# Optimization experiments

Hardware: AMD Instinct MI355X
Metric: run time of the kernel (lower is better)

The kernel has to match this reference:

```python
import jax, jax.numpy as jnp
import numpy as np

D, M, N = 1024, 16, 16384
H = D // M  # head dim = 64
C = 10.0    # tanh logit clipping


def setup_inputs() -> dict:
    key = jax.random.key(0)
    kb, kq, km, k1, k2, k3, k4 = jax.random.split(key, 7)
    def xavier(k, shape):
        # torch xavier_uniform: fan_in = prod(shape[1:]), fan_out = shape[0]*prod(shape[2:])
        fan_in = int(np.prod(shape[1:]))
        fan_out = shape[0] * int(np.prod(shape[2:]))
        bound = float(np.sqrt(6.0 / (fan_in + fan_out)))
        return jax.random.uniform(k, shape, jnp.float32, -bound, bound)
    return {
        "b": jax.random.normal(kb, (N, D), jnp.float32),
        "q_s_bar": jax.random.normal(kq, (D,), jnp.float32),
        "mask": jax.random.randint(km, (N,), 0, 2).astype(bool),
        "W_k_bar": xavier(k1, (M, H, D)),
        "W_v_bar": xavier(k2, (M, H, D)),
        "W_k": xavier(k3, (D, D)),
        "W_q": xavier(k4, (D, D)),
    }


def reference(b, q_s_bar, mask, W_k_bar, W_v_bar, W_k, W_q):
    # k_bar, v_bar: (N, M, H)  == matmul(W, b.t()).permute(2,0,1)
    k_bar = jnp.einsum('mhd,nd->nmh', W_k_bar, b)
    v_bar = jnp.einsum('mhd,nd->nmh', W_v_bar, b)
    k = b @ W_k.T                      # (N, D) == matmul(W_k, b.t()).t()
    q = q_s_bar.reshape(M, H)          # (M, H)
    # c_bar: (N, M, M) == matmul(k_bar, q.T) / sqrt(h)
    c_bar = jnp.einsum('nmh,gh->nmg', k_bar, q) / np.float32(np.sqrt(H))
    scores = jnp.where(mask[:, None, None], c_bar, -jnp.inf)
    attn = jax.nn.softmax(scores, axis=0)          # softmax over N
    # (N,M,M) @ (N,M,H) batched -> (N,M,H); view(N,-1).sum(0) -> (D,)
    q_s = jnp.einsum('nmg,ngh->nmh', attn, v_bar).reshape(N, D).sum(0)
    c = (k @ (W_q @ q_s)) / np.float32(np.sqrt(D))  # (N,)
    c = C * jnp.tanh(c)
    return jnp.where(mask, c, -jnp.inf)
```

## Files before the change

### kernel.cpp

```cpp
#include <hip/hip_runtime.h>
#include <math.h>
#include <float.h>

#define NN 16384
#define DD 1024
#define MM 16
#define HH 64
#define MG 256

typedef __attribute__((ext_vector_type(8))) short bh8;
typedef __attribute__((ext_vector_type(4))) float f32x4;

__device__ inline float bf2f(unsigned short u) {
    union { unsigned int i; float f; } v;
    v.i = ((unsigned int)u) << 16;
    return v.f;
}

__device__ inline unsigned short f2bf(float f) {
    union { float f; unsigned int i; } v;
    v.f = f;
    unsigned int r = v.i + 0x7FFFu + ((v.i >> 16) & 1u);
    return (unsigned short)(r >> 16);
}

__device__ inline float ld1(const void* p, long i, int isf) {
    return isf ? ((const float*)p)[i] : bf2f(((const unsigned short*)p)[i]);
}

__device__ inline float4 ld4(const void* p, long i, int isf) {
    if (isf) return *(const float4*)((const float*)p + i);
    ushort4 u = *(const ushort4*)((const unsigned short*)p + i);
    return make_float4(bf2f(u.x), bf2f(u.y), bf2f(u.z), bf2f(u.w));
}

__device__ inline bool get_mask(const unsigned char* mp, int n, int flag) {
    return flag ? (mp[n] != 0) : (mp[4 * n] != 0);
}

__device__ inline void gl_lds16(const void* g, void* l) {
    __builtin_amdgcn_global_load_lds(
        (const __attribute__((address_space(1))) unsigned int*)g,
        (__attribute__((address_space(3))) unsigned int*)l, 16, 0, 0);
}

__global__ void detect(const unsigned char* __restrict__ mp,
                       const unsigned char* __restrict__ bb, int* flags,
                       float* __restrict__ u, float* __restrict__ T) {
    int i = blockIdx.x * 256 + threadIdx.x;
    if (i < DD) u[i] = 0.f;
    float4 z = make_float4(0.f, 0.f, 0.f, 0.f);
#pragma unroll
    for (int j = 0; j < 4; j++) *(float4*)&T[(j * 16384 + i) * 4] = z;
    int v1 = ((i & 3) != 0 && mp[i] != 0) ? 1 : 0;
    unsigned char c = bb[4 * i + 1];
    bool expish = (c == 0x00) || (c == 0x80) || (c >= 0x30 && c <= 0x47) ||
                  (c >= 0xB0 && c <= 0xC7);
    int v2 = expish ? 0 : 1;
    unsigned long long b1 = __ballot(v1);
    unsigned long long b2 = __ballot(v2);
    if ((threadIdx.x & 63) == 0) {
        if (b1) atomicOr(&flags[0], 1);
        if (b2) atomicOr(&flags[1], 1);
    }
}

__global__ void fold_k(const void* __restrict__ Wkb, const void* __restrict__ qsb,
                       unsigned short* __restrict__ Abf, const int* __restrict__ flags) {
    __shared__ float q[DD];
    int isf = flags[1];
    int m = blockIdx.x;
    int d = blockIdx.y * 128 + threadIdx.x;
    for (int i = threadIdx.x; i < DD; i += 128) q[i] = ld1(qsb, i, isf);
    __syncthreads();
    float acc[MM];
#pragma unroll
    for (int g = 0; g < MM; g++) acc[g] = 0.f;
    for (int h = 0; h < HH; h++) {
        float w = ld1(Wkb, (long)(m * HH + h) * DD + d, isf);
#pragma unroll
        for (int g = 0; g < MM; g++) acc[g] += w * q[g * HH + h];
    }
#pragma unroll
    for (int g = 0; g < MM; g++)
        Abf[(long)(m * MM + g) * DD + d] = f2bf(acc[g] * 0.125f);
}

__global__ __launch_bounds__(256) void cvt_b(const void* __restrict__ bB,
                                             unsigned short* __restrict__ bbf,
                                             unsigned short* __restrict__ bT,
                                             const int* __restrict__ flags) {
    __shared__ unsigned short tl[2][32 * 68];
    const int isf = flags[1];
    const int t = threadIdx.x;
    const int n0 = blockIdx.x * 32;
    const int r = t >> 3, c8 = (t & 7) * 8;
    const int dT = t >> 2, ch = t & 3;
    const long gbase = (long)(n0 + r) * DD + c8;

    float cur[8], nxt[8];
    auto LOAD = [&](float* dst, int dt) {
        if (isf) {
            float4 v0 = *(const float4*)((const float*)bB + gbase + dt * 64);
            float4 v1 = *(const float4*)((const float*)bB + gbase + dt * 64 + 4);
            dst[0] = v0.x; dst[1] = v0.y; dst[2] = v0.z; dst[3] = v0.w;
            dst[4] = v1.x; dst[5] = v1.y; dst[6] = v1.z; dst[7] = v1.w;
        } else {
            bh8 v = *(const bh8*)((const unsigned short*)bB + gbase + dt * 64);
#pragma unroll
            for (int j = 0; j < 8; j++) dst[j] = bf2f((unsigned short)v[j]);
        }
    };

    LOAD(cur, 0);
#pragma unroll
    for (int dt = 0; dt < 16; dt++) {
        if (dt < 15) LOAD(nxt, dt + 1);
        bh8 o;
#pragma unroll
        for (int j = 0; j < 8; j++) o[j] = (short)f2bf(cur[j]);
        *(bh8*)&bbf[gbase + dt * 64] = o;
        unsigned short* row = &tl[dt & 1][r * 68 + c8];
        ushort4 lo, hi;
        lo.x = (unsigned short)o[0]; lo.y = (unsigned short)o[1];
        lo.z = (unsigned short)o[2]; lo.w = (unsigned short)o[3];
        hi.x = (unsigned short)o[4]; hi.y = (unsigned short)o[5];
        hi.z = (unsigned short)o[6]; hi.w = (unsigned short)o[7];
        *(ushort4*)row = lo;
        *(ushort4*)(row + 4) = hi;
        __syncthreads();
        bh8 y;
#pragma unroll
        for (int k = 0; k < 8; k++)
            y[k] = (short)tl[dt & 1][(ch * 8 + k) * 68 + dT];
        *(bh8*)&bT[(long)(dt * 64 + dT) * NN + n0 + ch * 8] = y;
#pragma unroll
        for (int j = 0; j < 8; j++) cur[j] = nxt[j];
    }
}

__global__ __launch_bounds__(256) void gemm_b_mfma(
    const unsigned short* __restrict__ Abf, const unsigned short* __restrict__ bbf,
    const unsigned char* __restrict__ mp, const int* __restrict__ flags,
    unsigned short* __restrict__ Cb) {
    __shared__ __align__(16) unsigned short As[128 * 64];
    __shared__ __align__(16) unsigned short Bs[64 * 64];
    int m0 = blockIdx.x * 128, n0 = blockIdx.y * 64;
    int t = threadIdx.x;
    int lane = t & 63, w = t >> 6;
    int wm = w >> 1, wn = w & 1;
    int r = lane & 15, q = lane >> 4;
    f32x4 acc[4][2] = {};
    for (int k0 = 0; k0 < DD; k0 += 64) {
#pragma unroll
        for (int i = 0; i < 4; i++) {
            int L = (i * 4 + w) * 64 + lane;
            int row = L >> 3, c = (L & 7) ^ (row & 7);
            gl_lds16(&Abf[(long)(m0 + row) * DD + k0 + c * 8], &As[(i * 4 + w) * 512]);
        }
#pragma unroll
        for (int i = 0; i < 2; i++) {
            int L = (i * 4 + w) * 64 + lane;
            int row = L >> 3, c = (L & 7) ^ (row & 7);
            gl_lds16(&bbf[(long)(n0 + row) * DD + k0 + c * 8], &Bs[(i * 4 + w) * 512]);
        }
        __syncthreads();
#pragma unroll
        for (int h = 0; h < 2; h++) {
            bh8 af[4], bfr[2];
#pragma unroll
            for (int fi = 0; fi < 4; fi++) {
                int row = wm * 64 + fi * 16 + r;
                int ck = (h * 4 + q) ^ (row & 7);
                af[fi] = *(const bh8*)&As[row * 64 + ck * 8];
            }
#pragma unroll
            for (int fj = 0; fj < 2; fj++) {
                int row = wn * 32 + fj * 16 + r;
                int ck = (h * 4 + q) ^ (row & 7);
                bfr[fj] = *(const bh8*)&Bs[row * 64 + ck * 8];
            }
#pragma unroll
            for (int fi = 0; fi < 4; fi++)
#pragma unroll
                for (int fj = 0; fj < 2; fj++)
                    acc[fi][fj] = __builtin_amdgcn_mfma_f32_16x16x32_bf16(
                        af[fi], bfr[fj], acc[fi][fj], 0, 0, 0);
        }
        __syncthreads();
    }
    int mflag = flags[0];
#pragma unroll
    for (int fj = 0; fj < 2; fj++) {
        int gn = n0 + wn * 32 + fj * 16 + r;
        float nb = get_mask(mp, gn, mflag) ? 0.f : -INFINITY;
#pragma unroll
        for (int fi = 0; fi < 4; fi++)
#pragma unroll
            for (int reg = 0; reg < 4; reg++) {
                int gm = m0 + wm * 64 + fi * 16 + q * 4 + reg;
                Cb[(long)gm * NN + gn] = f2bf(acc[fi][fj][reg] + nb);
            }
    }
}

__global__ __launch_bounds__(256) void softmax_f(const unsigned short* __restrict__ Cb,
                                                 unsigned short* __restrict__ P) {
    __shared__ float red[8];
    int mg = blockIdx.x, t = threadIdx.x;
    long base = (long)mg * NN;
    bh8 v[8];
#pragma unroll
    for (int j = 0; j < 8; j++) v[j] = *(const bh8*)&Cb[base + (j * 256 + t) * 8];
    float mx = -INFINITY;
#pragma unroll
    for (int j = 0; j < 8; j++)
#pragma unroll
        for (int e = 0; e < 8; e++) mx = fmaxf(mx, bf2f((unsigned short)v[j][e]));
#pragma unroll
    for (int off = 32; off; off >>= 1) mx = fmaxf(mx, __shfl_xor(mx, off, 64));
    if ((t & 63) == 0) red[t >> 6] = mx;
    __syncthreads();
    mx = fmaxf(fmaxf(red[0], red[1]), fmaxf(red[2], red[3]));
    float mxs = (mx == -INFINITY) ? 0.f : mx;
    float sm = 0.f;
#pragma unroll
    for (int j = 0; j < 8; j++)
#pragma unroll
        for (int e = 0; e < 8; e++) sm += expf(bf2f((unsigned short)v[j][e]) - mxs);
#pragma unroll
    for (int off = 32; off; off >>= 1) sm += __shfl_xor(sm, off, 64);
    if ((t & 63) == 0) red[4 + (t >> 6)] = sm;
    __syncthreads();
    sm = red[4] + red[5] + red[6] + red[7];
    float inv = (sm > 0.f) ? 1.0f / sm : 0.f;
#pragma unroll
    for (int j = 0; j < 8; j++) {
        bh8 o;
#pragma unroll
        for (int e = 0; e < 8; e++)
            o[e] = (short)f2bf(expf(bf2f((unsigned short)v[j][e]) - mxs) * inv);
        *(bh8*)&P[base + (j * 256 + t) * 8] = o;
    }
}

__global__ __launch_bounds__(256) void gemm_d_mfma(
    const unsigned short* __restrict__ P, const unsigned short* __restrict__ bT,
    float* __restrict__ T) {
    __shared__ __align__(16) unsigned short As[128 * 64];
    __shared__ __align__(16) unsigned short Bs[64 * 64];
    int m0 = blockIdx.x * 128, d0 = blockIdx.y * 64;
    long kbase = (long)blockIdx.z * 1024;
    int t = threadIdx.x;
    int lane = t & 63, w = t >> 6;
    int wm = w >> 1, wn = w & 1;
    int r = lane & 15, q = lane >> 4;
    f32x4 acc[4][2] = {};
    for (int k0 = 0; k0 < 1024; k0 += 64) {
#pragma unroll
        for (int i = 0; i < 4; i++) {
            int L = (i * 4 + w) * 64 + lane;
            int row = L >> 3, c = (L & 7) ^ (row & 7);
            gl_lds16(&P[(long)(m0 + row) * NN + kbase + k0 + c * 8], &As[(i * 4 + w) * 512]);
        }
#pragma unroll
        for (int i = 0; i < 2; i++) {
            int L = (i * 4 + w) * 64 + lane;
            int row = L >> 3, c = (L & 7) ^ (row & 7);
            gl_lds16(&bT[(long)(d0 + row) * NN + kbase + k0 + c * 8], &Bs[(i * 4 + w) * 512]);
        }
        __syncthreads();
#pragma unroll
        for (int h = 0; h < 2; h++) {
            bh8 af[4], bfr[2];
#pragma unroll
            for (int fi = 0; fi < 4; fi++) {
                int row = wm * 64 + fi * 16 + r;
                int ck = (h * 4 + q) ^ (row & 7);
                af[fi] = *(const bh8*)&As[row * 64 + ck * 8];
            }
#pragma unroll
            for (int fj = 0; fj < 2; fj++) {
                int row = wn * 32 + fj * 16 + r;
                int ck = (h * 4 + q) ^ (row & 7);
                bfr[fj] = *(const bh8*)&Bs[row * 64 + ck * 8];
            }
#pragma unroll
            for (int fi = 0; fi < 4; fi++)
#pragma unroll
                for (int fj = 0; fj < 2; fj++)
                    acc[fi][fj] = __builtin_amdgcn_mfma_f32_16x16x32_bf16(
                        af[fi], bfr[fj], acc[fi][fj], 0, 0, 0);
        }
        __syncthreads();
    }
#pragma unroll
    for (int fi = 0; fi < 4; fi++)
#pragma unroll
        for (int fj = 0; fj < 2; fj++)
#pragma unroll
            for (int reg = 0; reg < 4; reg++) {
                int gm = m0 + wm * 64 + fi * 16 + q * 4 + reg;
                int gd = d0 + wn * 32 + fj * 16 + r;
                atomicAdd(&T[(long)gm * DD + gd], acc[fi][fj][reg]);
            }
}

__global__ void fold_v(const void* __restrict__ Wvb, const float* __restrict__ T,
                       float* __restrict__ qs, const int* __restrict__ flags) {
    int isf = flags[1];
    int w = threadIdx.x >> 6, lane = threadIdx.x & 63;
    int o = blockIdx.x * 4 + w;
    int m = o >> 6, h = o & 63;
    float s = 0.f;
    for (int g = 0; g < MM; g++) {
        const float* Trow = T + (long)(m * MM + g) * DD;
        long wbase = (long)(g * HH + h) * DD;
#pragma unroll
        for (int k = 0; k < 4; k++) {
            int d = lane * 4 + k * 256;
            float4 tv = *(const float4*)&Trow[d];
            float4 wv = ld4(Wvb, wbase + d, isf);
            s += wv.x * tv.x + wv.y * tv.y + wv.z * tv.z + wv.w * tv.w;
        }
    }
    for (int off = 32; off; off >>= 1) s += __shfl_down(s, off, 64);
    if (lane == 0) qs[o] = s;
}

__global__ void matvec_rows(const void* __restrict__ W, const float* __restrict__ x,
                            float* __restrict__ y, const int* __restrict__ flags) {
    int isf = flags[1];
    int lane = threadIdx.x & 63;
    int r = blockIdx.x * 4 + (threadIdx.x >> 6);
    long base = (long)r * DD;
    float s = 0.f;
#pragma unroll
    for (int k = 0; k < 4; k++) {
        int j = lane * 4 + k * 256;
        float4 wv = ld4(W, base + j, isf);
        float4 xv = *(const float4*)&x[j];
        s += wv.x * xv.x + wv.y * xv.y + wv.z * xv.z + wv.w * xv.w;
    }
    for (int off = 32; off; off >>= 1) s += __shfl_down(s, off, 64);
    if (lane == 0) y[r] = s;
}

__global__ void matvec_col(const void* __restrict__ Wk, const float* __restrict__ w1,
                           float* __restrict__ u, const int* __restrict__ flags) {
    __shared__ float xs[16];
    int isf = flags[1];
    int d = blockIdx.x * 256 + threadIdx.x;
    int i0 = blockIdx.y * 16;
    if (threadIdx.x < 16) xs[threadIdx.x] = w1[i0 + threadIdx.x];
    __syncthreads();
    float s = 0.f;
#pragma unroll
    for (int ii = 0; ii < 16; ii++) s += ld1(Wk, (long)(i0 + ii) * DD + d, isf) * xs[ii];
    atomicAdd(&u[d], s);
}

__global__ void final_k(const unsigned short* __restrict__ bbf, const float* __restrict__ u,
                        const unsigned char* __restrict__ mp, const int* __restrict__ flags,
                        void* __restrict__ out) {
    int mflag = flags[0];
    int isf = flags[1];
    int n = blockIdx.x * 4 + (threadIdx.x >> 6);
    int lane = threadIdx.x & 63;
    const unsigned short* row = bbf + (long)n * DD;
    float s = 0.f;
#pragma unroll
    for (int k = 0; k < 4; k++) {
        int j = lane * 4 + k * 256;
        ushort4 v = *(const ushort4*)&row[j];
        float4 uu = *(const float4*)&u[j];
        s += bf2f(v.x) * uu.x + bf2f(v.y) * uu.y + bf2f(v.z) * uu.z + bf2f(v.w) * uu.w;
    }
    for (int off = 32; off; off >>= 1) s += __shfl_down(s, off, 64);
    if (lane == 0) {
        float c = 10.f * tanhf(s * (1.0f / 32.0f));
        bool mk = get_mask(mp, n, mflag);
        if (isf) {
            union { unsigned int i; float f; } vv;
            vv.i = mk ? (((unsigned int)f2bf(c)) << 16) : 0xFF7F0000u;
            ((float*)out)[n] = vv.f;
        } else {
            ((unsigned short*)out)[n] = mk ? f2bf(c) : (unsigned short)0xFF7F;
        }
    }
}

extern "C" void kernel_launch(void* const* d_in, const int* in_sizes, int n_in,
                              void* d_out, int out_size, void* d_ws, size_t ws_size,
                              hipStream_t stream) {
    const void* b = d_in[0];
    const void* qsb = d_in[1];
    const unsigned char* mp = (const unsigned char*)d_in[2];
    const void* Wkb = d_in[3];
    const void* Wvb = d_in[4];
    const void* Wk = d_in[5];
    const void* Wq = d_in[6];

    char* ws = (char*)d_ws;
    unsigned short* bbf = (unsigned short*)(ws);
    unsigned short* bT = (unsigned short*)(ws + (32u << 20));
    unsigned short* Cb = (unsigned short*)(ws + (64u << 20));
    unsigned short* P = (unsigned short*)(ws + (80u << 20));
    unsigned short* Abf = (unsigned short*)(ws + (88u << 20));
    float* T = (float*)(ws + (89u << 20));
    float* small = (float*)(ws + (90u << 20));
    float* qs = small;
    float* w1 = qs + 1024;
    float* u = w1 + 1024;
    int* flags = (int*)(u + 1024);

    hipMemsetAsync(flags, 0, 2 * sizeof(int), stream);

    detect<<<64, 256, 0, stream>>>(mp, (const unsigned char*)b, flags, u, T);
    fold_k<<<dim3(16, 8), 128, 0, stream>>>(Wkb, qsb, Abf, flags);
    cvt_b<<<512, 256, 0, stream>>>(b, bbf, bT, flags);
    gemm_b_mfma<<<dim3(2, 256), 256, 0, stream>>>(Abf, bbf, mp, flags, Cb);
    softmax_f<<<256, 256, 0, stream>>>(Cb, P);
    gemm_d_mfma<<<dim3(2, 16, 16), 256, 0, stream>>>(P, bT, T);
    fold_v<<<256, 256, 0, stream>>>(Wvb, T, qs, flags);
    matvec_rows<<<256, 256, 0, stream>>>(Wq, qs, w1, flags);
    matvec_col<<<dim3(4, 64), 256, 0, stream>>>(Wk, w1, u, flags);
    final_k<<<4096, 256, 0, stream>>>(bbf, u, mp, flags, d_out);
}
```

Measured before the change: 231.9 us.

## Double-buffer GEMM LDS tiles, split-K partials with reduce, wider softmax blocks

Both MFMA GEMMs now use two LDS buffers and issue the next k-tile's global-to-LDS loads before computing on the current tile, so memory latency can overlap with MFMA work. The split-K GEMM writes per-split partial results into a 16-slice buffer, and a new reduce kernel sums them. This replaces float atomics and removes the need to zero T in detect. Softmax now runs with 512 threads per row so each thread holds half as many registers. The cost is an extra kernel launch, a 16 MB partial buffer that must be written and read back, and twice the LDS per GEMM block, which may lower occupancy.

```diff
diff --git a/kernel.cpp b/kernel.cpp
--- a/kernel.cpp
+++ b/kernel.cpp
@@ -46,12 +46,9 @@
 
 __global__ void detect(const unsigned char* __restrict__ mp,
                        const unsigned char* __restrict__ bb, int* flags,
-                       float* __restrict__ u, float* __restrict__ T) {
+                       float* __restrict__ u) {
     int i = blockIdx.x * 256 + threadIdx.x;
     if (i < DD) u[i] = 0.f;
-    float4 z = make_float4(0.f, 0.f, 0.f, 0.f);
-#pragma unroll
-    for (int j = 0; j < 4; j++) *(float4*)&T[(j * 16384 + i) * 4] = z;
     int v1 = ((i & 3) != 0 && mp[i] != 0) ? 1 : 0;
     unsigned char c = bb[4 * i + 1];
     bool expish = (c == 0x00) || (c == 0x80) || (c >= 0x30 && c <= 0x47) ||
@@ -143,28 +140,35 @@
     const unsigned short* __restrict__ Abf, const unsigned short* __restrict__ bbf,
     const unsigned char* __restrict__ mp, const int* __restrict__ flags,
     unsigned short* __restrict__ Cb) {
-    __shared__ __align__(16) unsigned short As[128 * 64];
-    __shared__ __align__(16) unsigned short Bs[64 * 64];
+    __shared__ __align__(16) unsigned short As[2][128 * 64];
+    __shared__ __align__(16) unsigned short Bs[2][64 * 64];
     int m0 = blockIdx.x * 128, n0 = blockIdx.y * 64;
     int t = threadIdx.x;
     int lane = t & 63, w = t >> 6;
     int wm = w >> 1, wn = w & 1;
     int r = lane & 15, q = lane >> 4;
     f32x4 acc[4][2] = {};
-    for (int k0 = 0; k0 < DD; k0 += 64) {
+
+    auto STAGE = [&](int buf, int k0) {
 #pragma unroll
         for (int i = 0; i < 4; i++) {
             int L = (i * 4 + w) * 64 + lane;
             int row = L >> 3, c = (L & 7) ^ (row & 7);
-            gl_lds16(&Abf[(long)(m0 + row) * DD + k0 + c * 8], &As[(i * 4 + w) * 512]);
+            gl_lds16(&Abf[(long)(m0 + row) * DD + k0 + c * 8], &As[buf][(i * 4 + w) * 512]);
         }
 #pragma unroll
         for (int i = 0; i < 2; i++) {
             int L = (i * 4 + w) * 64 + lane;
             int row = L >> 3, c = (L & 7) ^ (row & 7);
-            gl_lds16(&bbf[(long)(n0 + row) * DD + k0 + c * 8], &Bs[(i * 4 + w) * 512]);
-        }
-        __syncthreads();
+            gl_lds16(&bbf[(long)(n0 + row) * DD + k0 + c * 8], &Bs[buf][(i * 4 + w) * 512]);
+        }
+    };
+
+    STAGE(0, 0);
+    __syncthreads();
+    int cur = 0;
+    for (int k0 = 0; k0 < DD; k0 += 64) {
+        if (k0 + 64 < DD) STAGE(cur ^ 1, k0 + 64);
 #pragma unroll
         for (int h = 0; h < 2; h++) {
             bh8 af[4], bfr[2];
@@ -172,13 +176,13 @@
             for (int fi = 0; fi < 4; fi++) {
                 int row = wm * 64 + fi * 16 + r;
                 int ck = (h * 4 + q) ^ (row & 7);
-                af[fi] = *(const bh8*)&As[row * 64 + ck * 8];
+                af[fi] = *(const bh8*)&As[cur][row * 64 + ck * 8];
             }
 #pragma unroll
             for (int fj = 0; fj < 2; fj++) {
                 int row = wn * 32 + fj * 16 + r;
                 int ck = (h * 4 + q) ^ (row & 7);
-                bfr[fj] = *(const bh8*)&Bs[row * 64 + ck * 8];
+                bfr[fj] = *(const bh8*)&Bs[cur][row * 64 + ck * 8];
             }
 #pragma unroll
             for (int fi = 0; fi < 4; fi++)
@@ -188,6 +192,7 @@
                         af[fi], bfr[fj], acc[fi][fj], 0, 0, 0);
         }
         __syncthreads();
+        cur ^= 1;
     }
     int mflag = flags[0];
 #pragma unroll
@@ -204,72 +209,84 @@
     }
 }
 
-__global__ __launch_bounds__(256) void softmax_f(const unsigned short* __restrict__ Cb,
+__global__ __launch_bounds__(512) void softmax_f(const unsigned short* __restrict__ Cb,
                                                  unsigned short* __restrict__ P) {
-    __shared__ float red[8];
+    __shared__ float red[16];
     int mg = blockIdx.x, t = threadIdx.x;
     long base = (long)mg * NN;
-    bh8 v[8];
-#pragma unroll
-    for (int j = 0; j < 8; j++) v[j] = *(const bh8*)&Cb[base + (j * 256 + t) * 8];
+    bh8 v[4];
+#pragma unroll
+    for (int j = 0; j < 4; j++) v[j] = *(const bh8*)&Cb[base + (j * 512 + t) * 8];
     float mx = -INFINITY;
 #pragma unroll
-    for (int j = 0; j < 8; j++)
+    for (int j = 0; j < 4; j++)
 #pragma unroll
         for (int e = 0; e < 8; e++) mx = fmaxf(mx, bf2f((unsigned short)v[j][e]));
 #pragma unroll
     for (int off = 32; off; off >>= 1) mx = fmaxf(mx, __shfl_xor(mx, off, 64));
     if ((t & 63) == 0) red[t >> 6] = mx;
     __syncthreads();
-    mx = fmaxf(fmaxf(red[0], red[1]), fmaxf(red[2], red[3]));
+    mx = red[0];
+#pragma unroll
+    for (int w2 = 1; w2 < 8; w2++) mx = fmaxf(mx, red[w2]);
     float mxs = (mx == -INFINITY) ? 0.f : mx;
     float sm = 0.f;
 #pragma unroll
-    for (int j = 0; j < 8; j++)
+    for (int j = 0; j < 4; j++)
 #pragma unroll
         for (int e = 0; e < 8; e++) sm += expf(bf2f((unsigned short)v[j][e]) - mxs);
 #pragma unroll
     for (int off = 32; off; off >>= 1) sm += __shfl_xor(sm, off, 64);
-    if ((t & 63) == 0) red[4 + (t >> 6)] = sm;
-    __syncthreads();
-    sm = red[4] + red[5] + red[6] + red[7];
+    if ((t & 63) == 0) red[8 + (t >> 6)] = sm;
+    __syncthreads();
+    sm = red[8];
+#pragma unroll
+    for (int w2 = 1; w2 < 8; w2++) sm += red[8 + w2];
     float inv = (sm > 0.f) ? 1.0f / sm : 0.f;
 #pragma unroll
-    for (int j = 0; j < 8; j++) {
+    for (int j = 0; j < 4; j++) {
         bh8 o;
 #pragma unroll
         for (int e = 0; e < 8; e++)
             o[e] = (short)f2bf(expf(bf2f((unsigned short)v[j][e]) - mxs) * inv);
-        *(bh8*)&P[base + (j * 256 + t) * 8] = o;
+        *(bh8*)&P[base + (j * 512 + t) * 8] = o;
     }
 }
 
 __global__ __launch_bounds__(256) void gemm_d_mfma(
     const unsigned short* __restrict__ P, const unsigned short* __restrict__ bT,
-    float* __restrict__ T) {
-    __shared__ __align__(16) unsigned short As[128 * 64];
-    __shared__ __align__(16) unsigned short Bs[64 * 64];
+    float* __restrict__ Tpart) {
+    __shared__ __align__(16) unsigned short As[2][128 * 64];
+    __shared__ __align__(16) unsigned short Bs[2][64 * 64];
     int m0 = blockIdx.x * 128, d0 = blockIdx.y * 64;
     long kbase = (long)blockIdx.z * 1024;
+    float* Cg = Tpart + (long)blockIdx.z * (MG * DD);
     int t = threadIdx.x;
     int lane = t & 63, w = t >> 6;
     int wm = w >> 1, wn = w & 1;
     int r = lane & 15, q = lane >> 4;
     f32x4 acc[4][2] = {};
-    for (int k0 = 0; k0 < 1024; k0 += 64) {
+
+    auto STAGE = [&](int buf, int k0) {
 #pragma unroll
         for (int i = 0; i < 4; i++) {
             int L = (i * 4 + w) * 64 + lane;
             int row = L >> 3, c = (L & 7) ^ (row & 7);
-            gl_lds16(&P[(long)(m0 + row) * NN + kbase + k0 + c * 8], &As[(i * 4 + w) * 512]);
+            gl_lds16(&P[(long)(m0 + row) * NN + kbase + k0 + c * 8], &As[buf][(i * 4 + w) * 512]);
         }
 #pragma unroll
         for (int i = 0; i < 2; i++) {
             int L = (i * 4 + w) * 64 + lane;
             int row = L >> 3, c = (L & 7) ^ (row & 7);
-            gl_lds16(&bT[(long)(d0 + row) * NN + kbase + k0 + c * 8], &Bs[(i * 4 + w) * 512]);
-        }
-        __syncthreads();
+            gl_lds16(&bT[(long)(d0 + row) * NN + kbase + k0 + c * 8], &Bs[buf][(i * 4 + w) * 512]);
+        }
+    };
+
+    STAGE(0, 0);
+    __syncthreads();
+    int cur = 0;
+    for (int k0 = 0; k0 < 1024; k0 += 64) {
+        if (k0 + 64 < 1024) STAGE(cur ^ 1, k0 + 64);
 #pragma unroll
         for (int h = 0; h < 2; h++) {
             bh8 af[4], bfr[2];
@@ -277,13 +294,13 @@
             for (int fi = 0; fi < 4; fi++) {
                 int row = wm * 64 + fi * 16 + r;
                 int ck = (h * 4 + q) ^ (row & 7);
-                af[fi] = *(const bh8*)&As[row * 64 + ck * 8];
+                af[fi] = *(const bh8*)&As[cur][row * 64 + ck * 8];
             }
 #pragma unroll
             for (int fj = 0; fj < 2; fj++) {
                 int row = wn * 32 + fj * 16 + r;
                 int ck = (h * 4 + q) ^ (row & 7);
-                bfr[fj] = *(const bh8*)&Bs[row * 64 + ck * 8];
+                bfr[fj] = *(const bh8*)&Bs[cur][row * 64 + ck * 8];
             }
 #pragma unroll
             for (int fi = 0; fi < 4; fi++)
@@ -293,6 +310,7 @@
                         af[fi], bfr[fj], acc[fi][fj], 0, 0, 0);
         }
         __syncthreads();
+        cur ^= 1;
     }
 #pragma unroll
     for (int fi = 0; fi < 4; fi++)
@@ -302,8 +320,19 @@
             for (int reg = 0; reg < 4; reg++) {
                 int gm = m0 + wm * 64 + fi * 16 + q * 4 + reg;
                 int gd = d0 + wn * 32 + fj * 16 + r;
-                atomicAdd(&T[(long)gm * DD + gd], acc[fi][fj][reg]);
-            }
+                Cg[(long)gm * DD + gd] = acc[fi][fj][reg];
+            }
+}
+
+__global__ void reduce_T(const float* __restrict__ Tpart, float* __restrict__ T) {
+    long i = (long)(blockIdx.x * 256 + threadIdx.x) * 4;
+    float4 s = make_float4(0.f, 0.f, 0.f, 0.f);
+#pragma unroll
+    for (int c = 0; c < 16; c++) {
+        float4 v = *(const float4*)&Tpart[(long)c * (MG * DD) + i];
+        s.x += v.x; s.y += v.y; s.z += v.z; s.w += v.w;
+    }
+    *(float4*)&T[i] = s;
 }
 
 __global__ void fold_v(const void* __restrict__ Wvb, const float* __restrict__ T,
@@ -405,10 +434,11 @@
     unsigned short* bbf = (unsigned short*)(ws);
     unsigned short* bT = (unsigned short*)(ws + (32u << 20));
     unsigned short* Cb = (unsigned short*)(ws + (64u << 20));
-    unsigned short* P = (unsigned short*)(ws + (80u << 20));
-    unsigned short* Abf = (unsigned short*)(ws + (88u << 20));
-    float* T = (float*)(ws + (89u << 20));
-    float* small = (float*)(ws + (90u << 20));
+    unsigned short* P = (unsigned short*)(ws + (72u << 20));
+    unsigned short* Abf = (unsigned short*)(ws + (80u << 20));
+    float* Tpart = (float*)(ws + (81u << 20));
+    float* T = (float*)(ws + (97u << 20));
+    float* small = (float*)(ws + (98u << 20));
     float* qs = small;
     float* w1 = qs + 1024;
     float* u = w1 + 1024;
@@ -416,12 +446,13 @@
 
     hipMemsetAsync(flags, 0, 2 * sizeof(int), stream);
 
-    detect<<<64, 256, 0, stream>>>(mp, (const unsigned char*)b, flags, u, T);
+    detect<<<64, 256, 0, stream>>>(mp, (const unsigned char*)b, flags, u);
     fold_k<<<dim3(16, 8), 128, 0, stream>>>(Wkb, qsb, Abf, flags);
     cvt_b<<<512, 256, 0, stream>>>(b, bbf, bT, flags);
     gemm_b_mfma<<<dim3(2, 256), 256, 0, stream>>>(Abf, bbf, mp, flags, Cb);
-    softmax_f<<<256, 256, 0, stream>>>(Cb, P);
-    gemm_d_mfma<<<dim3(2, 16, 16), 256, 0, stream>>>(P, bT, T);
+    softmax_f<<<256, 512, 0, stream>>>(Cb, P);
+    gemm_d_mfma<<<dim3(2, 16, 16), 256, 0, stream>>>(P, bT, Tpart);
+    reduce_T<<<256, 256, 0, stream>>>(Tpart, T);
     fold_v<<<256, 256, 0, stream>>>(Wvb, T, qs, flags);
     matvec_rows<<<256, 256, 0, stream>>>(Wq, qs, w1, flags);
     matvec_col<<<dim3(4, 64), 256, 0, stream>>>(Wk, w1, u, flags);
```

New measurement: 230.2 us. Within noise of the previous version (-0.7%).

## Fuse tail matvec kernels into one persistent kernel with grid barriers

Applied to the files above, without the earlier changes.

Replaces the atomic fp32 accumulation into T with per-split bf16 partial outputs, which are then reduced inside a new fused tail kernel. The tail kernel chains the reduction, fold_v, the Wq matvec, the Wk column matvec and the final score computation, separated by software grid barriers, so four kernel launches and the zeroing of T go away. Softmax now runs with 512 threads per block. The risks are deadlock if all 256 blocks are not co-resident and extra precision loss from storing the partial sums in bf16.

```diff
diff --git a/kernel.cpp b/kernel.cpp
--- a/kernel.cpp
+++ b/kernel.cpp
@@ -46,12 +46,9 @@
 
 __global__ void detect(const unsigned char* __restrict__ mp,
                        const unsigned char* __restrict__ bb, int* flags,
-                       float* __restrict__ u, float* __restrict__ T) {
+                       float* __restrict__ u) {
     int i = blockIdx.x * 256 + threadIdx.x;
     if (i < DD) u[i] = 0.f;
-    float4 z = make_float4(0.f, 0.f, 0.f, 0.f);
-#pragma unroll
-    for (int j = 0; j < 4; j++) *(float4*)&T[(j * 16384 + i) * 4] = z;
     int v1 = ((i & 3) != 0 && mp[i] != 0) ? 1 : 0;
     unsigned char c = bb[4 * i + 1];
     bool expish = (c == 0x00) || (c == 0x80) || (c >= 0x30 && c <= 0x47) ||
@@ -204,53 +201,58 @@
     }
 }
 
-__global__ __launch_bounds__(256) void softmax_f(const unsigned short* __restrict__ Cb,
+__global__ __launch_bounds__(512) void softmax_f(const unsigned short* __restrict__ Cb,
                                                  unsigned short* __restrict__ P) {
-    __shared__ float red[8];
+    __shared__ float red[16];
     int mg = blockIdx.x, t = threadIdx.x;
     long base = (long)mg * NN;
-    bh8 v[8];
-#pragma unroll
-    for (int j = 0; j < 8; j++) v[j] = *(const bh8*)&Cb[base + (j * 256 + t) * 8];
+    bh8 v[4];
+#pragma unroll
+    for (int j = 0; j < 4; j++) v[j] = *(const bh8*)&Cb[base + (j * 512 + t) * 8];
     float mx = -INFINITY;
 #pragma unroll
-    for (int j = 0; j < 8; j++)
+    for (int j = 0; j < 4; j++)
 #pragma unroll
         for (int e = 0; e < 8; e++) mx = fmaxf(mx, bf2f((unsigned short)v[j][e]));
 #pragma unroll
     for (int off = 32; off; off >>= 1) mx = fmaxf(mx, __shfl_xor(mx, off, 64));
     if ((t & 63) == 0) red[t >> 6] = mx;
     __syncthreads();
-    mx = fmaxf(fmaxf(red[0], red[1]), fmaxf(red[2], red[3]));
+    mx = red[0];
+#pragma unroll
+    for (int w2 = 1; w2 < 8; w2++) mx = fmaxf(mx, red[w2]);
     float mxs = (mx == -INFINITY) ? 0.f : mx;
     float sm = 0.f;
 #pragma unroll
-    for (int j = 0; j < 8; j++)
+    for (int j = 0; j < 4; j++)
 #pragma unroll
         for (int e = 0; e < 8; e++) sm += expf(bf2f((unsigned short)v[j][e]) - mxs);
 #pragma unroll
     for (int off = 32; off; off >>= 1) sm += __shfl_xor(sm, off, 64);
-    if ((t & 63) == 0) red[4 + (t >> 6)] = sm;
+    if ((t & 63) == 0) red[8 + (t >> 6)] = sm;
     __syncthreads();
-    sm = red[4] + red[5] + red[6] + red[7];
+    sm = red[8];
+#pragma unroll
+    for (int w2 = 1; w2 < 8; w2++) sm += red[8 + w2];
     float inv = (sm > 0.f) ? 1.0f / sm : 0.f;
 #pragma unroll
-    for (int j = 0; j < 8; j++) {
+    for (int j = 0; j < 4; j++) {
         bh8 o;
 #pragma unroll
         for (int e = 0; e < 8; e++)
             o[e] = (short)f2bf(expf(bf2f((unsigned short)v[j][e]) - mxs) * inv);
-        *(bh8*)&P[base + (j * 256 + t) * 8] = o;
+        *(bh8*)&P[base + (j * 512 + t) * 8] = o;
     }
 }
 
 __global__ __launch_bounds__(256) void gemm_d_mfma(
     const unsigned short* __restrict__ P, const unsigned short* __restrict__ bT,
-    float* __restrict__ T) {
+    unsigned short* __restrict__ Tpart) {
     __shared__ __align__(16) unsigned short As[128 * 64];
     __shared__ __align__(16) unsigned short Bs[64 * 64];
     int m0 = blockIdx.x * 128, d0 = blockIdx.y * 64;
     long kbase = (long)blockIdx.z * 1024;
+    unsigned short* Cg = Tpart + (long)blockIdx.z * (MG * DD);
     int t = threadIdx.x;
     int lane = t & 63, w = t >> 6;
     int wm = w >> 1, wn = w & 1;
@@ -302,90 +304,125 @@
             for (int reg = 0; reg < 4; reg++) {
                 int gm = m0 + wm * 64 + fi * 16 + q * 4 + reg;
                 int gd = d0 + wn * 32 + fj * 16 + r;
-                atomicAdd(&T[(long)gm * DD + gd], acc[fi][fj][reg]);
-            }
-}
-
-__global__ void fold_v(const void* __restrict__ Wvb, const float* __restrict__ T,
-                       float* __restrict__ qs, const int* __restrict__ flags) {
-    int isf = flags[1];
-    int w = threadIdx.x >> 6, lane = threadIdx.x & 63;
-    int o = blockIdx.x * 4 + w;
-    int m = o >> 6, h = o & 63;
-    float s = 0.f;
-    for (int g = 0; g < MM; g++) {
-        const float* Trow = T + (long)(m * MM + g) * DD;
-        long wbase = (long)(g * HH + h) * DD;
+                Cg[(long)gm * DD + gd] = f2bf(acc[fi][fj][reg]);
+            }
+}
+
+__device__ inline void gbar(int* bars, int idx, int nb) {
+    __syncthreads();
+    if (threadIdx.x == 0) {
+        __threadfence();
+        __hip_atomic_fetch_add(&bars[idx], 1, __ATOMIC_RELEASE, __HIP_MEMORY_SCOPE_AGENT);
+        while (__hip_atomic_load(&bars[idx], __ATOMIC_ACQUIRE, __HIP_MEMORY_SCOPE_AGENT) < nb)
+            __builtin_amdgcn_s_sleep(2);
+        __threadfence();
+    }
+    __syncthreads();
+}
+
+__global__ __launch_bounds__(512) void tail_k(
+    const unsigned short* __restrict__ Tpart, float* __restrict__ T,
+    const void* __restrict__ Wvb, float* __restrict__ qs,
+    const void* __restrict__ Wq, float* __restrict__ w1,
+    const void* __restrict__ Wk, float* __restrict__ u,
+    const unsigned short* __restrict__ bbf,
+    const unsigned char* __restrict__ mp, const int* __restrict__ flags,
+    int* bars, void* __restrict__ out) {
+    __shared__ float xs[16];
+    int b = blockIdx.x, t = threadIdx.x;
+    int w = t >> 6, lane = t & 63;
+    int isf = flags[1], mflag = flags[0];
+
+    if (t < 256) {
+        long i = (long)(b * 256 + t) * 4;
+        float4 s = make_float4(0.f, 0.f, 0.f, 0.f);
+#pragma unroll
+        for (int c = 0; c < 16; c++) {
+            ushort4 v = *(const ushort4*)&Tpart[(long)c * (MG * DD) + i];
+            s.x += bf2f(v.x); s.y += bf2f(v.y); s.z += bf2f(v.z); s.w += bf2f(v.w);
+        }
+        *(float4*)&T[i] = s;
+    }
+    gbar(bars, 0, 256);
+
+    if (w < 4) {
+        int o = b * 4 + w;
+        int m = o >> 6, h = o & 63;
+        float s = 0.f;
+        for (int g = 0; g < MM; g++) {
+            const float* Trow = T + (long)(m * MM + g) * DD;
+            long wbase = (long)(g * HH + h) * DD;
+#pragma unroll
+            for (int k = 0; k < 4; k++) {
+                int d = lane * 4 + k * 256;
+                float4 tv = *(const float4*)&Trow[d];
+                float4 wv = ld4(Wvb, wbase + d, isf);
+                s += wv.x * tv.x + wv.y * tv.y + wv.z * tv.z + wv.w * tv.w;
+            }
+        }
+        for (int off = 32; off; off >>= 1) s += __shfl_down(s, off, 64);
+        if (lane == 0) qs[o] = s;
+    }
+    gbar(bars, 1, 256);
+
+    if (w < 4) {
+        int r = b * 4 + w;
+        long base = (long)r * DD;
+        float s = 0.f;
 #pragma unroll
         for (int k = 0; k < 4; k++) {
-            int d = lane * 4 + k * 256;
-            float4 tv = *(const float4*)&Trow[d];
-            float4 wv = ld4(Wvb, wbase + d, isf);
-            s += wv.x * tv.x + wv.y * tv.y + wv.z * tv.z + wv.w * tv.w;
-        }
-    }
-    for (int off = 32; off; off >>= 1) s += __shfl_down(s, off, 64);
-    if (lane == 0) qs[o] = s;
-}
-
-__global__ void matvec_rows(const void* __restrict__ W, const float* __restrict__ x,
-                            float* __restrict__ y, const int* __restrict__ flags) {
-    int isf = flags[1];
-    int lane = threadIdx.x & 63;
-    int r = blockIdx.x * 4 + (threadIdx.x >> 6);
-    long base = (long)r * DD;
-    float s = 0.f;
-#pragma unroll
-    for (int k = 0; k < 4; k++) {
-        int j = lane * 4 + k * 256;
-        float4 wv = ld4(W, base + j, isf);
-        float4 xv = *(const float4*)&x[j];
-        s += wv.x * xv.x + wv.y * xv.y + wv.z * xv.z + wv.w * xv.w;
-    }
-    for (int off = 32; off; off >>= 1) s += __shfl_down(s, off, 64);
-    if (lane == 0) y[r] = s;
-}
-
-__global__ void matvec_col(const void* __restrict__ Wk, const float* __restrict__ w1,
-                           float* __restrict__ u, const int* __restrict__ flags) {
-    __shared__ float xs[16];
-    int isf = flags[1];
-    int d = blockIdx.x * 256 + threadIdx.x;
-    int i0 = blockIdx.y * 16;
-    if (threadIdx.x < 16) xs[threadIdx.x] = w1[i0 + threadIdx.x];
-    __syncthreads();
-    float s = 0.f;
-#pragma unroll
-    for (int ii = 0; ii < 16; ii++) s += ld1(Wk, (long)(i0 + ii) * DD + d, isf) * xs[ii];
-    atomicAdd(&u[d], s);
-}
-
-__global__ void final_k(const unsigned short* __restrict__ bbf, const float* __restrict__ u,
-                        const unsigned char* __restrict__ mp, const int* __restrict__ flags,
-                        void* __restrict__ out) {
-    int mflag = flags[0];
-    int isf = flags[1];
-    int n = blockIdx.x * 4 + (threadIdx.x >> 6);
-    int lane = threadIdx.x & 63;
-    const unsigned short* row = bbf + (long)n * DD;
-    float s = 0.f;
-#pragma unroll
-    for (int k = 0; k < 4; k++) {
-        int j = lane * 4 + k * 256;
-        ushort4 v = *(const ushort4*)&row[j];
-        float4 uu = *(const float4*)&u[j];
-        s += bf2f(v.x) * uu.x + bf2f(v.y) * uu.y + bf2f(v.z) * uu.z + bf2f(v.w) * uu.w;
-    }
-    for (int off = 32; off; off >>= 1) s += __shfl_down(s, off, 64);
-    if (lane == 0) {
-        float c = 10.f * tanhf(s * (1.0f / 32.0f));
-        bool mk = get_mask(mp, n, mflag);
-        if (isf) {
-            union { unsigned int i; float f; } vv;
-            vv.i = mk ? (((unsigned int)f2bf(c)) << 16) : 0xFF7F0000u;
-            ((float*)out)[n] = vv.f;
-        } else {
-            ((unsigned short*)out)[n] = mk ? f2bf(c) : (unsigned short)0xFF7F;
+            int j = lane * 4 + k * 256;
+            float4 wv = ld4(Wq, base + j, isf);
+            float4 xv = *(const float4*)&qs[j];
+            s += wv.x * xv.x + wv.y * xv.y + wv.z * xv.z + wv.w * xv.w;
+        }
+        for (int off = 32; off; off >>= 1) s += __shfl_down(s, off, 64);
+        if (lane == 0) w1[r] = s;
+    }
+    gbar(bars, 2, 256);
+
+    {
+        int bx = b & 3, by = b >> 2;
+        if (t < 16) xs[t] = w1[by * 16 + t];
+        __syncthreads();
+        if (t < 256) {
+            int d = bx * 256 + t;
+            float s = 0.f;
+#pragma unroll
+            for (int ii = 0; ii < 16; ii++)
+                s += ld1(Wk, (long)(by * 16 + ii) * DD + d, isf) * xs[ii];
+            atomicAdd(&u[d], s);
+        }
+    }
+    gbar(bars, 3, 256);
+
+    float4 u0 = *(const float4*)&u[lane * 4];
+    float4 u1 = *(const float4*)&u[lane * 4 + 256];
+    float4 u2 = *(const float4*)&u[lane * 4 + 512];
+    float4 u3 = *(const float4*)&u[lane * 4 + 768];
+#pragma unroll
+    for (int i = 0; i < 8; i++) {
+        int n = b * 8 + w + i * 2048;
+        const unsigned short* row = bbf + (long)n * DD;
+        ushort4 v0 = *(const ushort4*)&row[lane * 4];
+        ushort4 v1 = *(const ushort4*)&row[lane * 4 + 256];
+        ushort4 v2 = *(const ushort4*)&row[lane * 4 + 512];
+        ushort4 v3 = *(const ushort4*)&row[lane * 4 + 768];
+        float s = bf2f(v0.x) * u0.x + bf2f(v0.y) * u0.y + bf2f(v0.z) * u0.z + bf2f(v0.w) * u0.w
+                + bf2f(v1.x) * u1.x + bf2f(v1.y) * u1.y + bf2f(v1.z) * u1.z + bf2f(v1.w) * u1.w
+                + bf2f(v2.x) * u2.x + bf2f(v2.y) * u2.y + bf2f(v2.z) * u2.z + bf2f(v2.w) * u2.w
+                + bf2f(v3.x) * u3.x + bf2f(v3.y) * u3.y + bf2f(v3.z) * u3.z + bf2f(v3.w) * u3.w;
+        for (int off = 32; off; off >>= 1) s += __shfl_down(s, off, 64);
+        if (lane == 0) {
+            float c = 10.f * tanhf(s * (1.0f / 32.0f));
+            bool mk = get_mask(mp, n, mflag);
+            if (isf) {
+                union { unsigned int ui; float f; } vv;
+                vv.ui = mk ? (((unsigned int)f2bf(c)) << 16) : 0xFF7F0000u;
+                ((float*)out)[n] = vv.f;
+            } else {
+                ((unsigned short*)out)[n] = mk ? f2bf(c) : (unsigned short)0xFF7F;
+            }
         }
     }
 }
@@ -405,6 +442,7 @@
     unsigned short* bbf = (unsigned short*)(ws);
     unsigned short* bT = (unsigned short*)(ws + (32u << 20));
     unsigned short* Cb = (unsigned short*)(ws + (64u << 20));
+    unsigned short* Tpart = (unsigned short*)(ws + (72u << 20));
     unsigned short* P = (unsigned short*)(ws + (80u << 20));
     unsigned short* Abf = (unsigned short*)(ws + (88u << 20));
     float* T = (float*)(ws + (89u << 20));
@@ -413,17 +451,16 @@
     float* w1 = qs + 1024;
     float* u = w1 + 1024;
     int* flags = (int*)(u + 1024);
-
-    hipMemsetAsync(flags, 0, 2 * sizeof(int), stream);
-
-    detect<<<64, 256, 0, stream>>>(mp, (const unsigned char*)b, flags, u, T);
+    int* bars = flags + 2;
+
+    hipMemsetAsync(flags, 0, 16 * sizeof(int), stream);
+
+    detect<<<64, 256, 0, stream>>>(mp, (const unsigned char*)b, flags, u);
     fold_k<<<dim3(16, 8), 128, 0, stream>>>(Wkb, qsb, Abf, flags);
     cvt_b<<<512, 256, 0, stream>>>(b, bbf, bT, flags);
     gemm_b_mfma<<<dim3(2, 256), 256, 0, stream>>>(Abf, bbf, mp, flags, Cb);
-    softmax_f<<<256, 256, 0, stream>>>(Cb, P);
-    gemm_d_mfma<<<dim3(2, 16, 16), 256, 0, stream>>>(P, bT, T);
-    fold_v<<<256, 256, 0, stream>>>(Wvb, T, qs, flags);
-    matvec_rows<<<256, 256, 0, stream>>>(Wq, qs, w1, flags);
-    matvec_col<<<dim3(4, 64), 256, 0, stream>>>(Wk, w1, u, flags);
-    final_k<<<4096, 256, 0, stream>>>(bbf, u, mp, flags, d_out);
-}
+    softmax_f<<<256, 512, 0, stream>>>(Cb, P);
+    gemm_d_mfma<<<dim3(2, 16, 16), 256, 0, stream>>>(P, bT, Tpart);
+    tail_k<<<256, 512, 0, stream>>>(Tpart, T, Wvb, qs, Wq, w1, Wk, u,
+                                    bbf, mp, flags, bars, d_out);
+}
```

Result: slower. 316.4 us (+36.4%).

## Replace split-K atomics with bf16 partials plus reduction, XCD-aware block remap

Applied to the files above, without the earlier changes.

The split-K GEMM over N now writes bf16 partial tiles to a workspace buffer instead of doing fp32 atomicAdd into T. A new reduce kernel sums the 16 partials into T, which also removes the zeroing of T in detect. Both MFMA GEMMs use a 1D grid with a block-index remap so that blocks sharing an operand slice land on the same XCD, aiming for better L2 reuse. The softmax is relaunched with 512 threads per row. Rounding the partials to bf16 adds precision loss, and the change adds one kernel launch.

```diff
diff --git a/kernel.cpp b/kernel.cpp
--- a/kernel.cpp
+++ b/kernel.cpp
@@ -46,12 +46,9 @@
 
 __global__ void detect(const unsigned char* __restrict__ mp,
                        const unsigned char* __restrict__ bb, int* flags,
-                       float* __restrict__ u, float* __restrict__ T) {
+                       float* __restrict__ u) {
     int i = blockIdx.x * 256 + threadIdx.x;
     if (i < DD) u[i] = 0.f;
-    float4 z = make_float4(0.f, 0.f, 0.f, 0.f);
-#pragma unroll
-    for (int j = 0; j < 4; j++) *(float4*)&T[(j * 16384 + i) * 4] = z;
     int v1 = ((i & 3) != 0 && mp[i] != 0) ? 1 : 0;
     unsigned char c = bb[4 * i + 1];
     bool expish = (c == 0x00) || (c == 0x80) || (c >= 0x30 && c <= 0x47) ||
@@ -145,7 +142,9 @@
     unsigned short* __restrict__ Cb) {
     __shared__ __align__(16) unsigned short As[128 * 64];
     __shared__ __align__(16) unsigned short Bs[64 * 64];
-    int m0 = blockIdx.x * 128, n0 = blockIdx.y * 64;
+    int i = blockIdx.x;
+    int nsl = (i & 7) | ((i >> 4) << 3);
+    int m0 = ((i >> 3) & 1) * 128, n0 = nsl * 64;
     int t = threadIdx.x;
     int lane = t & 63, w = t >> 6;
     int wm = w >> 1, wn = w & 1;
@@ -153,16 +152,16 @@
     f32x4 acc[4][2] = {};
     for (int k0 = 0; k0 < DD; k0 += 64) {
 #pragma unroll
-        for (int i = 0; i < 4; i++) {
-            int L = (i * 4 + w) * 64 + lane;
+        for (int i2 = 0; i2 < 4; i2++) {
+            int L = (i2 * 4 + w) * 64 + lane;
             int row = L >> 3, c = (L & 7) ^ (row & 7);
-            gl_lds16(&Abf[(long)(m0 + row) * DD + k0 + c * 8], &As[(i * 4 + w) * 512]);
-        }
-#pragma unroll
-        for (int i = 0; i < 2; i++) {
-            int L = (i * 4 + w) * 64 + lane;
+            gl_lds16(&Abf[(long)(m0 + row) * DD + k0 + c * 8], &As[(i2 * 4 + w) * 512]);
+        }
+#pragma unroll
+        for (int i2 = 0; i2 < 2; i2++) {
+            int L = (i2 * 4 + w) * 64 + lane;
             int row = L >> 3, c = (L & 7) ^ (row & 7);
-            gl_lds16(&bbf[(long)(n0 + row) * DD + k0 + c * 8], &Bs[(i * 4 + w) * 512]);
+            gl_lds16(&bbf[(long)(n0 + row) * DD + k0 + c * 8], &Bs[(i2 * 4 + w) * 512]);
         }
         __syncthreads();
 #pragma unroll
@@ -204,53 +203,63 @@
     }
 }
 
-__global__ __launch_bounds__(256) void softmax_f(const unsigned short* __restrict__ Cb,
+__global__ __launch_bounds__(512) void softmax_f(const unsigned short* __restrict__ Cb,
                                                  unsigned short* __restrict__ P) {
-    __shared__ float red[8];
+    __shared__ float red[16];
     int mg = blockIdx.x, t = threadIdx.x;
     long base = (long)mg * NN;
-    bh8 v[8];
-#pragma unroll
-    for (int j = 0; j < 8; j++) v[j] = *(const bh8*)&Cb[base + (j * 256 + t) * 8];
+    bh8 v[4];
+#pragma unroll
+    for (int j = 0; j < 4; j++) v[j] = *(const bh8*)&Cb[base + (j * 512 + t) * 8];
     float mx = -INFINITY;
 #pragma unroll
-    for (int j = 0; j < 8; j++)
+    for (int j = 0; j < 4; j++)
 #pragma unroll
         for (int e = 0; e < 8; e++) mx = fmaxf(mx, bf2f((unsigned short)v[j][e]));
 #pragma unroll
     for (int off = 32; off; off >>= 1) mx = fmaxf(mx, __shfl_xor(mx, off, 64));
     if ((t & 63) == 0) red[t >> 6] = mx;
     __syncthreads();
-    mx = fmaxf(fmaxf(red[0], red[1]), fmaxf(red[2], red[3]));
+    mx = red[0];
+#pragma unroll
+    for (int w2 = 1; w2 < 8; w2++) mx = fmaxf(mx, red[w2]);
     float mxs = (mx == -INFINITY) ? 0.f : mx;
     float sm = 0.f;
 #pragma unroll
-    for (int j = 0; j < 8; j++)
+    for (int j = 0; j < 4; j++)
 #pragma unroll
         for (int e = 0; e < 8; e++) sm += expf(bf2f((unsigned short)v[j][e]) - mxs);
 #pragma unroll
     for (int off = 32; off; off >>= 1) sm += __shfl_xor(sm, off, 64);
-    if ((t & 63) == 0) red[4 + (t >> 6)] = sm;
+    if ((t & 63) == 0) red[8 + (t >> 6)] = sm;
     __syncthreads();
-    sm = red[4] + red[5] + red[6] + red[7];
+    sm = red[8];
+#pragma unroll
+    for (int w2 = 1; w2 < 8; w2++) sm += red[8 + w2];
     float inv = (sm > 0.f) ? 1.0f / sm : 0.f;
 #pragma unroll
-    for (int j = 0; j < 8; j++) {
+    for (int j = 0; j < 4; j++) {
         bh8 o;
 #pragma unroll
         for (int e = 0; e < 8; e++)
             o[e] = (short)f2bf(expf(bf2f((unsigned short)v[j][e]) - mxs) * inv);
-        *(bh8*)&P[base + (j * 256 + t) * 8] = o;
+        *(bh8*)&P[base + (j * 512 + t) * 8] = o;
     }
 }
 
 __global__ __launch_bounds__(256) void gemm_d_mfma(
     const unsigned short* __restrict__ P, const unsigned short* __restrict__ bT,
-    float* __restrict__ T) {
+    unsigned short* __restrict__ Tpart) {
     __shared__ __align__(16) unsigned short As[128 * 64];
     __shared__ __align__(16) unsigned short Bs[64 * 64];
-    int m0 = blockIdx.x * 128, d0 = blockIdx.y * 64;
-    long kbase = (long)blockIdx.z * 1024;
+    int i = blockIdx.x;
+    int xcd = i & 7, k = i >> 3;
+    int z = xcd + 8 * (k & 1);
+    int inner = k >> 1;
+    int d0 = (inner >> 1) * 64;
+    int m0 = (inner & 1) * 128;
+    long kbase = (long)z * 1024;
+    unsigned short* Cg = Tpart + (long)z * (MG * DD);
     int t = threadIdx.x;
     int lane = t & 63, w = t >> 6;
     int wm = w >> 1, wn = w & 1;
@@ -258,16 +267,16 @@
     f32x4 acc[4][2] = {};
     for (int k0 = 0; k0 < 1024; k0 += 64) {
 #pragma unroll
-        for (int i = 0; i < 4; i++) {
-            int L = (i * 4 + w) * 64 + lane;
+        for (int i2 = 0; i2 < 4; i2++) {
+            int L = (i2 * 4 + w) * 64 + lane;
             int row = L >> 3, c = (L & 7) ^ (row & 7);
-            gl_lds16(&P[(long)(m0 + row) * NN + kbase + k0 + c * 8], &As[(i * 4 + w) * 512]);
-        }
-#pragma unroll
-        for (int i = 0; i < 2; i++) {
-            int L = (i * 4 + w) * 64 + lane;
+            gl_lds16(&P[(long)(m0 + row) * NN + kbase + k0 + c * 8], &As[(i2 * 4 + w) * 512]);
+        }
+#pragma unroll
+        for (int i2 = 0; i2 < 2; i2++) {
+            int L = (i2 * 4 + w) * 64 + lane;
             int row = L >> 3, c = (L & 7) ^ (row & 7);
-            gl_lds16(&bT[(long)(d0 + row) * NN + kbase + k0 + c * 8], &Bs[(i * 4 + w) * 512]);
+            gl_lds16(&bT[(long)(d0 + row) * NN + kbase + k0 + c * 8], &Bs[(i2 * 4 + w) * 512]);
         }
         __syncthreads();
 #pragma unroll
@@ -302,8 +311,21 @@
             for (int reg = 0; reg < 4; reg++) {
                 int gm = m0 + wm * 64 + fi * 16 + q * 4 + reg;
                 int gd = d0 + wn * 32 + fj * 16 + r;
-                atomicAdd(&T[(long)gm * DD + gd], acc[fi][fj][reg]);
-            }
+                Cg[(long)gm * DD + gd] = f2bf(acc[fi][fj][reg]);
+            }
+}
+
+__global__ void reduce_T(const unsigned short* __restrict__ Tpart, float* __restrict__ T) {
+    long i = (long)(blockIdx.x * 256 + threadIdx.x) * 8;
+    float s[8] = {};
+#pragma unroll
+    for (int c = 0; c < 16; c++) {
+        bh8 v = *(const bh8*)&Tpart[(long)c * (MG * DD) + i];
+#pragma unroll
+        for (int j = 0; j < 8; j++) s[j] += bf2f((unsigned short)v[j]);
+    }
+    *(float4*)&T[i] = make_float4(s[0], s[1], s[2], s[3]);
+    *(float4*)&T[i + 4] = make_float4(s[4], s[5], s[6], s[7]);
 }
 
 __global__ void fold_v(const void* __restrict__ Wvb, const float* __restrict__ T,
@@ -405,6 +427,7 @@
     unsigned short* bbf = (unsigned short*)(ws);
     unsigned short* bT = (unsigned short*)(ws + (32u << 20));
     unsigned short* Cb = (unsigned short*)(ws + (64u << 20));
+    unsigned short* Tpart = (unsigned short*)(ws + (72u << 20));
     unsigned short* P = (unsigned short*)(ws + (80u << 20));
     unsigned short* Abf = (unsigned short*)(ws + (88u << 20));
     float* T = (float*)(ws + (89u << 20));
@@ -416,12 +439,13 @@
 
     hipMemsetAsync(flags, 0, 2 * sizeof(int), stream);
 
-    detect<<<64, 256, 0, stream>>>(mp, (const unsigned char*)b, flags, u, T);
+    detect<<<64, 256, 0, stream>>>(mp, (const unsigned char*)b, flags, u);
     fold_k<<<dim3(16, 8), 128, 0, stream>>>(Wkb, qsb, Abf, flags);
     cvt_b<<<512, 256, 0, stream>>>(b, bbf, bT, flags);
-    gemm_b_mfma<<<dim3(2, 256), 256, 0, stream>>>(Abf, bbf, mp, flags, Cb);
-    softmax_f<<<256, 256, 0, stream>>>(Cb, P);
-    gemm_d_mfma<<<dim3(2, 16, 16), 256, 0, stream>>>(P, bT, T);
+    gemm_b_mfma<<<512, 256, 0, stream>>>(Abf, bbf, mp, flags, Cb);
+    softmax_f<<<256, 512, 0, stream>>>(Cb, P);
+    gemm_d_mfma<<<512, 256, 0, stream>>>(P, bT, Tpart);
+    reduce_T<<<128, 256, 0, stream>>>(Tpart, T);
     fold_v<<<256, 256, 0, stream>>>(Wvb, T, qs, flags);
     matvec_rows<<<256, 256, 0, stream>>>(Wq, qs, w1, flags);
     matvec_col<<<dim3(4, 64), 256, 0, stream>>>(Wk, w1, u, flags);
```

After: 220.5 us. 1.05x faster.
